# Kernel optimization log

Measured on AMD Instinct MI355X. Metric: run time of the kernel, lower is better.

## Reference

```python
import jax, jax.numpy as jnp
import numpy as np

B, N, C = 4, 256, 256
FH, FW = 100, 152
IMG_H, IMG_W = 800, 1216
SCALE = 0.125          # feature stride 8
POOL, RATIO = 7, 2     # MultiScaleRoIAlign output_size / sampling_ratio
NUM_CLASSES = 91
SCORE_T, NMS_T = 0.05, 0.5
PRE_NMS, DETS = 1024, 100   # fixed-size candidate set for jit-able NMS
WX, WY, WW, WH = 10.0, 10.0, 5.0, 5.0   # bbox_reg_weights
BBOX_CLIP = float(np.log(1000.0 / 16.0))
MIN_SIZE = 1e-2


def setup_inputs():
    key = jax.random.key(0)
    k = jax.random.split(key, 8)
    features = jax.random.normal(k[0], (B, C, FH, FW), jnp.float32)
    p = jax.random.uniform(k[1], (B, N, 4), jnp.float32)
    x1 = jnp.minimum(p[..., 0], p[..., 1]) * (IMG_W - 1.0)
    x2 = jnp.maximum(p[..., 0], p[..., 1]) * (IMG_W - 1.0) + 1.0
    y1 = jnp.minimum(p[..., 2], p[..., 3]) * (IMG_H - 1.0)
    y2 = jnp.maximum(p[..., 2], p[..., 3]) * (IMG_H - 1.0) + 1.0
    proposals = jnp.stack([x1, y1, x2, y2], -1)
    Din = C * POOL * POOL
    W6 = jax.random.normal(k[2], (Din, 1024), jnp.float32) / np.sqrt(Din)
    b6 = jnp.zeros((1024,), jnp.float32)
    W7 = jax.random.normal(k[3], (1024, 1024), jnp.float32) / np.sqrt(1024)
    b7 = jnp.zeros((1024,), jnp.float32)
    Wc = jax.random.normal(k[4], (1024, NUM_CLASSES), jnp.float32) / np.sqrt(1024)
    bc = jnp.zeros((NUM_CLASSES,), jnp.float32)
    Wb = jax.random.normal(k[5], (1024, NUM_CLASSES * 4), jnp.float32) / np.sqrt(1024)
    bb = jnp.zeros((NUM_CLASSES * 4,), jnp.float32)
    return {"features": features, "proposals": proposals, "W6": W6, "b6": b6,
            "W7": W7, "b7": b7, "Wc": Wc, "bc": bc, "Wb": Wb, "bb": bb}


def roi_align(feat, rois, bidx):
    # feat [B,C,H,W]; rois [R,4] in image coords; bidx [R] image index.
    R = rois.shape[0]
    x1, y1 = rois[:, 0] * SCALE, rois[:, 1] * SCALE
    x2, y2 = rois[:, 2] * SCALE, rois[:, 3] * SCALE
    rw = jnp.maximum(x2 - x1, 1.0)
    rh = jnp.maximum(y2 - y1, 1.0)
    off = (jnp.arange(RATIO, dtype=feat.dtype) + 0.5) / RATIO
    grid = (jnp.arange(POOL, dtype=feat.dtype)[:, None] + off[None, :]).reshape(-1)  # [POOL*RATIO]
    gx = jnp.clip(x1[:, None] + (rw / POOL)[:, None] * grid[None, :], 0.0, FW - 1.0)  # [R,14]
    gy = jnp.clip(y1[:, None] + (rh / POOL)[:, None] * grid[None, :], 0.0, FH - 1.0)
    y0 = jnp.floor(gy); x0 = jnp.floor(gx)
    ly = gy - y0; lx = gx - x0
    y0i = jnp.clip(y0, 0, FH - 1).astype(jnp.int32)
    y1i = jnp.clip(y0 + 1.0, 0, FH - 1).astype(jnp.int32)
    x0i = jnp.clip(x0, 0, FW - 1).astype(jnp.int32)
    x1i = jnp.clip(x0 + 1.0, 0, FW - 1).astype(jnp.int32)
    b = bidx[:, None, None]
    def g(yi, xi):  # -> [R, Py, Px, C]
        return feat[b, :, yi[:, :, None], xi[:, None, :]]
    v = ((1 - ly)[:, :, None] * (1 - lx)[:, None, :])[..., None] * g(y0i, x0i) \
      + ((1 - ly)[:, :, None] * lx[:, None, :])[..., None] * g(y0i, x1i) \
      + (ly[:, :, None] * (1 - lx)[:, None, :])[..., None] * g(y1i, x0i) \
      + (ly[:, :, None] * lx[:, None, :])[..., None] * g(y1i, x1i)
    v = v.reshape(R, POOL, RATIO, POOL, RATIO, C).mean((2, 4))  # avg over samples per bin
    return jnp.transpose(v, (0, 3, 1, 2)).reshape(R, C * POOL * POOL)  # channel-major flatten


def decode(deltas, rois):
    # BoxCoder.decode with weights (10,10,5,5); deltas [R,K*4] -> [R,K,4]
    w = rois[:, 2] - rois[:, 0]
    h = rois[:, 3] - rois[:, 1]
    cx = rois[:, 0] + 0.5 * w
    cy = rois[:, 1] + 0.5 * h
    d = deltas.reshape(deltas.shape[0], -1, 4)
    dx, dy = d[..., 0] / WX, d[..., 1] / WY
    dw = jnp.minimum(d[..., 2] / WW, BBOX_CLIP)
    dh = jnp.minimum(d[..., 3] / WH, BBOX_CLIP)
    pcx = dx * w[:, None] + cx[:, None]
    pcy = dy * h[:, None] + cy[:, None]
    pw = jnp.exp(dw) * w[:, None]
    ph = jnp.exp(dh) * h[:, None]
    return jnp.stack([pcx - 0.5 * pw, pcy - 0.5 * ph, pcx + 0.5 * pw, pcy + 0.5 * ph], -1)


def box_iou(a, b):
    area_a = (a[:, 2] - a[:, 0]) * (a[:, 3] - a[:, 1])
    area_b = (b[:, 2] - b[:, 0]) * (b[:, 3] - b[:, 1])
    lt = jnp.maximum(a[:, None, :2], b[None, :, :2])
    rb = jnp.minimum(a[:, None, 2:], b[None, :, 2:])
    wh = jnp.clip(rb - lt, 0.0)
    inter = wh[..., 0] * wh[..., 1]
    return inter / (area_a[:, None] + area_b[None, :] - inter + 1e-9)


def _post(boxes, scores):
    # per-image: boxes [N,K1,4], scores [N,K1] (background already dropped)
    n = boxes.shape[0]
    k1 = boxes.shape[1]
    fb = boxes.reshape(-1, 4)
    fs = scores.reshape(-1)
    labels = jnp.tile(jnp.arange(1, k1 + 1, dtype=jnp.int32), n)
    ws = fb[:, 2] - fb[:, 0]
    hs = fb[:, 3] - fb[:, 1]
    valid = (fs > SCORE_T) & (ws >= MIN_SIZE) & (hs >= MIN_SIZE)
    vals, idx = jax.lax.top_k(jnp.where(valid, fs, -1.0), PRE_NMS)
    cb = fb[idx]
    cl = labels[idx]
    # batched per-class NMS via class offset trick
    ob = cb + (cl.astype(cb.dtype) * (max(IMG_H, IMG_W) + 2.0))[:, None]
    iou = box_iou(ob, ob)
    ar = jnp.arange(PRE_NMS)
    def body(i, keep):
        sup = keep[i] & (iou[i] > NMS_T) & (ar > i)
        return keep & jnp.logical_not(sup)
    keep = jax.lax.fori_loop(0, PRE_NMS, body, vals > SCORE_T)
    sv, oidx = jax.lax.top_k(jnp.where(keep, vals, -1.0), DETS)
    m = sv > SCORE_T
    out_boxes = jnp.where(m[:, None], cb[oidx], 0.0)
    out_scores = jnp.where(m, sv, 0.0)
    out_labels = jnp.where(m, cl[oidx], 0)
    return out_boxes, out_scores, out_labels


def _forward(features, proposals, W6, b6, W7, b7, Wc, bc, Wb, bb):
    rois = proposals.reshape(-1, 4)                     # [R,4]
    bidx = jnp.repeat(jnp.arange(B, dtype=jnp.int32), N)
    x = roi_align(features, rois, bidx)                 # [R, C*49]
    x = jax.nn.relu(x @ W6 + b6)                        # TwoMLPHead fc6
    x = jax.nn.relu(x @ W7 + b7)                        # fc7
    logits = x @ Wc + bc                                # FastRCNNPredictor
    deltas = x @ Wb + bb
    boxes = decode(deltas, rois)                        # [R,K,4]
    boxes = jnp.stack([jnp.clip(boxes[..., 0], 0.0, IMG_W),
                       jnp.clip(boxes[..., 1], 0.0, IMG_H),
                       jnp.clip(boxes[..., 2], 0.0, IMG_W),
                       jnp.clip(boxes[..., 3], 0.0, IMG_H)], -1)
    scores = jax.nn.softmax(logits, -1)
    boxes = boxes[:, 1:].reshape(B, N, NUM_CLASSES - 1, 4)   # drop background class
    scores = scores[:, 1:].reshape(B, N, NUM_CLASSES - 1)
    return jax.vmap(_post)(boxes, scores)


def reference(features, proposals, W6, b6, W7, b7, Wc, bc, Wb, bb):
    # returns (boxes [B,100,4], scores [B,100], labels [B,100])
    return _forward(features, proposals, W6, b6, W7, b7, Wc, bc, Wb, bb)
```

## Files before the change

kernel.cpp:

```cpp
#include <hip/hip_runtime.h>
#include <hip/hip_bf16.h>
#include <stdint.h>

#define B_    4
#define N_    256
#define C_    256
#define FH_   100
#define FW_   152
#define P_HW  (FH_*FW_)
#define NCLS  91
#define CAND  23040
#define DIN   12544
#define PRE   1024

typedef unsigned long long u64;
typedef unsigned int u32;
typedef unsigned short u16;
typedef __attribute__((ext_vector_type(8))) _Float16 half8;
typedef __attribute__((ext_vector_type(8))) short short8;
typedef __attribute__((ext_vector_type(4))) float f32x4;

__device__ inline u16 h2bits(_Float16 h) { return *reinterpret_cast<u16*>(&h); }

__device__ inline void split2(float v, u16& b0, u16& b1) {
  _Float16 h0 = (_Float16)v;
  float r = v - (float)h0;
  _Float16 h1 = (_Float16)r;
  b0 = h2bits(h0); b1 = h2bits(h1);
}

__device__ inline void gload_lds16(const void* g, void* l) {
  __builtin_amdgcn_global_load_lds(
      (const __attribute__((address_space(1))) void*)g,
      (__attribute__((address_space(3))) void*)l, 16, 0, 0);
}

__global__ void k_transpose(const float* __restrict__ in, float* __restrict__ out) {
  __shared__ float t[32][33];
  int b  = blockIdx.z;
  int c0 = blockIdx.y * 32;
  int p0 = blockIdx.x * 32;
  int tx = threadIdx.x & 31, ty = threadIdx.x >> 5;
  const float* inb = in  + (size_t)b * C_ * P_HW;
  float*       ob  = out + (size_t)b * P_HW * C_;
  #pragma unroll
  for (int q = 0; q < 4; q++)
    t[ty + q*8][tx] = inb[(size_t)(c0 + ty + q*8) * P_HW + p0 + tx];
  __syncthreads();
  #pragma unroll
  for (int q = 0; q < 4; q++)
    ob[(size_t)(p0 + ty + q*8) * C_ + c0 + tx] = t[tx][ty + q*8];
}

__global__ void k_packs(const float* __restrict__ W7, u16* __restrict__ W7t,
                        const float* __restrict__ Wc, const float* __restrict__ Wb,
                        const float* __restrict__ bc, const float* __restrict__ bb,
                        u16* __restrict__ Wcatt, float* __restrict__ bcat) {
  int bid = blockIdx.x;
  int tid = threadIdx.x;
  if (bid < 512) {
    int idx = bid * 256 + tid;
    int col = idx & 1023, ko = idx >> 10;
    short8 c0v, c1v;
    #pragma unroll
    for (int e = 0; e < 8; e++) {
      float w = W7[(size_t)(ko*8 + e)*1024 + col] * 128.0f;
      u16 h0, h1;
      split2(w, h0, h1);
      c0v[e] = (short)h0; c1v[e] = (short)h1;
    }
    *reinterpret_cast<short8*>(W7t + ((size_t)ko*1024 + col)*8)         = c0v;
    *reinterpret_cast<short8*>(W7t + ((size_t)(128 + ko)*1024 + col)*8) = c1v;
  } else {
    int idx = (bid - 512) * 256 + tid;
    int col = idx & 511, ko = idx >> 9;
    short8 c0v, c1v;
    #pragma unroll
    for (int e = 0; e < 8; e++) {
      int k = ko*8 + e;
      float w = 0.f;
      if (col < 91)       w = Wc[(size_t)k*91 + col];
      else if (col < 455) w = Wb[(size_t)k*364 + (col - 91)];
      w *= 128.0f;
      u16 h0, h1;
      split2(w, h0, h1);
      c0v[e] = (short)h0; c1v[e] = (short)h1;
    }
    *reinterpret_cast<short8*>(Wcatt + ((size_t)ko*512 + col)*8)         = c0v;
    *reinterpret_cast<short8*>(Wcatt + ((size_t)(128 + ko)*512 + col)*8) = c1v;
    if (idx < 512) {
      float bv = 0.f;
      if (idx < 91)       bv = bc[idx];
      else if (idx < 455) bv = bb[idx - 91];
      bcat[idx] = bv;
    }
  }
}

__global__ __launch_bounds__(256, 8) void k_roialign(const float* __restrict__ featT,
                                                     const float* __restrict__ props,
                                                     u16* __restrict__ Xs) {
  __shared__ float sPW[196][8];
  __shared__ float cellv[32][51];
  int bid = blockIdx.x;
  int xcd = bid & 7;
  int b = xcd >> 1;
  int n = ((bid >> 3) << 1) | (xcd & 1);
  int r = (b << 8) | n;
  int tid = threadIdx.x;

  float x1 = props[r*4+0], y1 = props[r*4+1];
  float x2 = props[r*4+2], y2 = props[r*4+3];
  float x1s = x1 * 0.125f, y1s = y1 * 0.125f;
  float x2s = x2 * 0.125f, y2s = y2 * 0.125f;
  float rw = fmaxf(x2s - x1s, 1.0f);
  float rh = fmaxf(y2s - y1s, 1.0f);
  float rwd = rw / 7.0f, rhd = rh / 7.0f;

  if (tid < 196) {
    int cell = tid >> 2, s = tid & 3;
    int py = cell / 7, px = cell % 7;
    int sy = s >> 1, sx = s & 1;
    float gqy = (float)py + 0.25f + 0.5f * (float)sy;
    float gqx = (float)px + 0.25f + 0.5f * (float)sx;
    float gy = fminf(fmaxf(y1s + rhd * gqy, 0.0f), 99.0f);
    float gx = fminf(fmaxf(x1s + rwd * gqx, 0.0f), 151.0f);
    float y0f = floorf(gy), x0f = floorf(gx);
    float ly = gy - y0f, lx = gx - x0f;
    int y0i = (int)y0f;
    int y1i = (int)fminf(y0f + 1.0f, 99.0f);
    int x0i = (int)x0f;
    int x1i = (int)fminf(x0f + 1.0f, 151.0f);
    sPW[tid][0] = __int_as_float((y0i * FW_ + x0i) * 256);
    sPW[tid][1] = __int_as_float((y0i * FW_ + x1i) * 256);
    sPW[tid][2] = __int_as_float((y1i * FW_ + x0i) * 256);
    sPW[tid][3] = __int_as_float((y1i * FW_ + x1i) * 256);
    sPW[tid][4] = (1.f-ly)*(1.f-lx);
    sPW[tid][5] = (1.f-ly)*lx;
    sPW[tid][6] = ly*(1.f-lx);
    sPW[tid][7] = ly*lx;
  }
  __syncthreads();

  int c32 = tid & 31;
  int slot = tid >> 5;
  const size_t PLS = (size_t)(DIN/8) * 1024 * 8;

  for (int g = 0; g < 8; g++) {
    const float* fb = featT + (size_t)b * P_HW * C_ + g*32 + c32;
    for (int cell = slot; cell < 49; cell += 8) {
      float acc = 0.f;
      #pragma unroll
      for (int s = 0; s < 4; s++) {
        int cs = cell*4 + s;
        float4 pv = *(const float4*)&sPW[cs][0];
        float4 wv = *(const float4*)&sPW[cs][4];
        acc += wv.x * fb[__float_as_int(pv.x)]
             + wv.y * fb[__float_as_int(pv.y)]
             + wv.z * fb[__float_as_int(pv.z)]
             + wv.w * fb[__float_as_int(pv.w)];
      }
      cellv[c32][cell] = acc * 4.0f;
    }
    __syncthreads();
    if (tid < 196) {
      short8 v0, v1;
      #pragma unroll
      for (int e = 0; e < 8; e++) {
        int kl = tid*8 + e;
        int chl = kl / 49;
        int cell = kl - chl*49;
        float v = cellv[chl][cell];
        u16 h0, h1;
        split2(v, h0, h1);
        v0[e] = (short)h0; v1[e] = (short)h1;
      }
      size_t cg = (size_t)g*196 + tid;
      size_t base = (cg * 1024 + r) * 8;
      *reinterpret_cast<short8*>(Xs + base)       = v0;
      *reinterpret_cast<short8*>(Xs + PLS + base) = v1;
    }
    __syncthreads();
  }
}

__global__ __launch_bounds__(512) void k_gemm_f16(
    const u16* __restrict__ As, const float* __restrict__ Bw,
    float* __restrict__ part, int kg, int nsteps, int nct, int outw,
    size_t sstride) {
  __shared__ __align__(16) char lds[65536];
  int tid = threadIdx.x;
  int wid = tid >> 6, lane = tid & 63;
  int l15 = lane & 15, lq = lane >> 4;
  int bid = blockIdx.x;
  int z = bid & 7, xy = bid >> 3;
  int col0 = (xy % nct) * 128, row0 = (xy / nct) * 128;
  int wr = wid >> 2, wc = wid & 3;
  int kbase0 = z * nsteps * 32;

  auto STAGE = [&](int s, int bsel) {
    int kb = kbase0 + s * 32;
    char* dst = lds + bsel * 32768;
    #pragma unroll
    for (int j = 0; j < 4; j++) {
      int cid = tid + j*512;
      const char* src;
      if (j < 2) {
        int pl = cid >> 9;
        int kc = (cid >> 7) & 3, rr = cid & 127;
        src = (const char*)(As + ((size_t)(pl*kg + (kb>>3) + kc)*1024 + row0 + rr)*8);
      } else {
        int cid2 = cid - 1024;
        int kk = cid2 >> 5, c4 = cid2 & 31;
        int col = (c4*4) ^ (((kk >> 3) & 1) << 4);
        src = (const char*)(Bw + (size_t)(kb + kk)*outw + col0 + col);
      }
      gload_lds16(src, dst + (size_t)cid*16);
    }
  };

  f32x4 acc[4][2];
  #pragma unroll
  for (int i = 0; i < 4; i++)
    #pragma unroll
    for (int j = 0; j < 2; j++)
      #pragma unroll
      for (int q = 0; q < 4; q++) acc[i][j][q] = 0.f;

  STAGE(0, 0);
  for (int s = 0; s < nsteps; s++) {
    int cur = s & 1;
    if (s + 1 < nsteps) {
      STAGE(s + 1, cur ^ 1);
      asm volatile("s_waitcnt vmcnt(4)" ::: "memory");
    } else {
      asm volatile("s_waitcnt vmcnt(0)" ::: "memory");
    }
    __builtin_amdgcn_s_barrier();
    __builtin_amdgcn_sched_barrier(0);

    const u16*   Alds = (const u16*)(lds + cur * 32768);
    const float* Blds = (const float*)(lds + cur * 32768 + 16384);

    half8 af[2][4];
    #pragma unroll
    for (int pl = 0; pl < 2; pl++)
      #pragma unroll
      for (int fr = 0; fr < 4; fr++) {
        int chunk = (pl*4 + lq)*128 + wr*64 + fr*16 + l15;
        af[pl][fr] = *reinterpret_cast<const half8*>(&Alds[(size_t)chunk*8]);
      }
    int cxor = (lq & 1) << 4;
    #pragma unroll
    for (int fc = 0; fc < 2; fc++) {
      int colx = (wc*32 + fc*16 + l15) ^ cxor;
      half8 b0, b1;
      #pragma unroll
      for (int j = 0; j < 8; j++) {
        float w = Blds[(lq*8 + j)*128 + colx] * 128.0f;
        _Float16 h0 = (_Float16)w;
        float rres = w - (float)h0;
        b0[j] = h0; b1[j] = (_Float16)rres;
      }
      #pragma unroll
      for (int fr = 0; fr < 4; fr++) {
        acc[fr][fc] = __builtin_amdgcn_mfma_f32_16x16x32_f16(af[0][fr], b0, acc[fr][fc], 0, 0, 0);
        acc[fr][fc] = __builtin_amdgcn_mfma_f32_16x16x32_f16(af[1][fr], b0, acc[fr][fc], 0, 0, 0);
        acc[fr][fc] = __builtin_amdgcn_mfma_f32_16x16x32_f16(af[0][fr], b1, acc[fr][fc], 0, 0, 0);
      }
    }
    __builtin_amdgcn_sched_barrier(0);
    asm volatile("s_waitcnt lgkmcnt(0)" ::: "memory");
    __builtin_amdgcn_s_barrier();
  }

  float* pp = part + (size_t)z * sstride;
  #pragma unroll
  for (int fr = 0; fr < 4; fr++)
    #pragma unroll
    for (int fc = 0; fc < 2; fc++) {
      int col = col0 + wc*32 + fc*16 + l15;
      #pragma unroll
      for (int rr = 0; rr < 4; rr++) {
        int row = row0 + wr*64 + fr*16 + lq*4 + rr;
        pp[(size_t)row*outw + col] = acc[fr][fc][rr];
      }
    }
}

__global__ __launch_bounds__(512) void k_gemm_f16b(
    const u16* __restrict__ As, const u16* __restrict__ Bt,
    float* __restrict__ part, int kgA, int kgB, int nsteps, int nct, int outw,
    size_t sstride) {
  __shared__ __align__(16) char lds[65536];
  int tid = threadIdx.x;
  int wid = tid >> 6, lane = tid & 63;
  int l15 = lane & 15, lq = lane >> 4;
  int bid = blockIdx.x;
  int z = bid & 7, xy = bid >> 3;
  int col0 = (xy % nct) * 128, row0 = (xy / nct) * 128;
  int wr = wid >> 2, wc = wid & 3;
  int kbase0 = z * nsteps * 32;

  auto STAGE = [&](int s, int bsel) {
    int kb = kbase0 + s * 32;
    char* dst = lds + bsel * 32768;
    #pragma unroll
    for (int j = 0; j < 4; j++) {
      int cid = tid + j*512;
      const char* src;
      if (j < 2) {
        int pl = cid >> 9;
        int kc = (cid >> 7) & 3, rr = cid & 127;
        src = (const char*)(As + ((size_t)(pl*kgA + (kb>>3) + kc)*1024 + row0 + rr)*8);
      } else {
        int cid2 = cid - 1024;
        int pl = cid2 >> 9;
        int kc = (cid2 >> 7) & 3, cc = cid2 & 127;
        src = (const char*)(Bt + ((size_t)(pl*kgB + (kb>>3) + kc)*outw + col0 + cc)*8);
      }
      gload_lds16(src, dst + (size_t)cid*16);
    }
  };

  f32x4 acc[4][2];
  #pragma unroll
  for (int i = 0; i < 4; i++)
    #pragma unroll
    for (int j = 0; j < 2; j++)
      #pragma unroll
      for (int q = 0; q < 4; q++) acc[i][j][q] = 0.f;

  STAGE(0, 0);
  for (int s = 0; s < nsteps; s++) {
    int cur = s & 1;
    if (s + 1 < nsteps) {
      STAGE(s + 1, cur ^ 1);
      asm volatile("s_waitcnt vmcnt(4)" ::: "memory");
    } else {
      asm volatile("s_waitcnt vmcnt(0)" ::: "memory");
    }
    __builtin_amdgcn_s_barrier();
    __builtin_amdgcn_sched_barrier(0);

    const u16* Alds = (const u16*)(lds + cur * 32768);
    const u16* Blds = (const u16*)(lds + cur * 32768 + 16384);

    half8 af[2][4];
    #pragma unroll
    for (int pl = 0; pl < 2; pl++)
      #pragma unroll
      for (int fr = 0; fr < 4; fr++) {
        int chunk = (pl*4 + lq)*128 + wr*64 + fr*16 + l15;
        af[pl][fr] = *reinterpret_cast<const half8*>(&Alds[(size_t)chunk*8]);
      }
    #pragma unroll
    for (int fc = 0; fc < 2; fc++) {
      int cc = wc*32 + fc*16 + l15;
      half8 b0 = *reinterpret_cast<const half8*>(&Blds[(size_t)((0*4 + lq)*128 + cc)*8]);
      half8 b1 = *reinterpret_cast<const half8*>(&Blds[(size_t)((1*4 + lq)*128 + cc)*8]);
      #pragma unroll
      for (int fr = 0; fr < 4; fr++) {
        acc[fr][fc] = __builtin_amdgcn_mfma_f32_16x16x32_f16(af[0][fr], b0, acc[fr][fc], 0, 0, 0);
        acc[fr][fc] = __builtin_amdgcn_mfma_f32_16x16x32_f16(af[1][fr], b0, acc[fr][fc], 0, 0, 0);
        acc[fr][fc] = __builtin_amdgcn_mfma_f32_16x16x32_f16(af[0][fr], b1, acc[fr][fc], 0, 0, 0);
      }
    }
    __builtin_amdgcn_sched_barrier(0);
    asm volatile("s_waitcnt lgkmcnt(0)" ::: "memory");
    __builtin_amdgcn_s_barrier();
  }

  float* pp = part + (size_t)z * sstride;
  #pragma unroll
  for (int fr = 0; fr < 4; fr++)
    #pragma unroll
    for (int fc = 0; fc < 2; fc++) {
      int col = col0 + wc*32 + fc*16 + l15;
      #pragma unroll
      for (int rr = 0; rr < 4; rr++) {
        int row = row0 + wr*64 + fr*16 + lq*4 + rr;
        pp[(size_t)row*outw + col] = acc[fr][fc][rr];
      }
    }
}

__global__ void k_reduce_split(const float* __restrict__ part,
                               const float* __restrict__ bias,
                               u16* __restrict__ ys) {
  int idx = blockIdx.x * 256 + threadIdx.x;
  int row = idx >> 7, cg = idx & 127;
  float4 s0 = {0,0,0,0}, s1 = {0,0,0,0};
  #pragma unroll
  for (int s = 0; s < 8; s++) {
    const float4* p = (const float4*)(part + (size_t)s*1048576 + (size_t)row*1024 + cg*8);
    float4 a = p[0], b = p[1];
    s0.x += a.x; s0.y += a.y; s0.z += a.z; s0.w += a.w;
    s1.x += b.x; s1.y += b.y; s1.z += b.z; s1.w += b.w;
  }
  float v[8] = {s0.x, s0.y, s0.z, s0.w, s1.x, s1.y, s1.z, s1.w};
  short8 o0, o1;
  #pragma unroll
  for (int e = 0; e < 8; e++) {
    float x = v[e] * (1.0f/2048.0f) + bias[cg*8 + e];
    x = fmaxf(x, 0.f) * 16.0f;
    u16 h0, h1;
    split2(x, h0, h1);
    o0[e] = (short)h0; o1[e] = (short)h1;
  }
  size_t base = ((size_t)cg * 1024 + row) * 8;
  *reinterpret_cast<short8*>(ys + base)               = o0;
  *reinterpret_cast<short8*>(ys + (size_t)1048576 + base) = o1;
}

__global__ __launch_bounds__(128) void k_headfin(const float* __restrict__ part,
                                                 const float* __restrict__ bcat,
                                                 const float* __restrict__ props,
                                                 float* __restrict__ cboxes,
                                                 u64* __restrict__ keys) {
  __shared__ float sc[512];
  __shared__ float red[128];
  int r = blockIdx.x;
  int j = threadIdx.x;
  int c0 = j * 4;
  float4 v = {0.f, 0.f, 0.f, 0.f};
  #pragma unroll
  for (int s = 0; s < 8; s++) {
    float4 p = *(const float4*)(part + (size_t)s*524288 + (size_t)r*512 + c0);
    v.x += p.x; v.y += p.y; v.z += p.z; v.w += p.w;
  }
  float4 bz = *(const float4*)(bcat + c0);
  sc[c0+0] = v.x * (1.0f/2048.0f) + bz.x;
  sc[c0+1] = v.y * (1.0f/2048.0f) + bz.y;
  sc[c0+2] = v.z * (1.0f/2048.0f) + bz.z;
  sc[c0+3] = v.w * (1.0f/2048.0f) + bz.w;
  __syncthreads();

  float lg = (j < NCLS) ? sc[j] : -3.4e38f;
  red[j] = lg;
  __syncthreads();
  for (int s = 64; s > 0; s >>= 1) {
    if (j < s) red[j] = fmaxf(red[j], red[j+s]);
    __syncthreads();
  }
  float mx = red[0];
  __syncthreads();
  float e = (j < NCLS) ? expf(lg - mx) : 0.f;
  red[j] = e;
  __syncthreads();
  for (int s = 64; s > 0; s >>= 1) {
    if (j < s) red[j] += red[j+s];
    __syncthreads();
  }
  float p = e / red[0];
  if (j >= 1 && j < NCLS) {
    float px1 = props[r*4+0], py1 = props[r*4+1];
    float px2 = props[r*4+2], py2 = props[r*4+3];
    float w = px2 - px1, h = py2 - py1;
    float cx = px1 + 0.5f*w, cy = py1 + 0.5f*h;
    float d0 = sc[91 + j*4 + 0];
    float d1 = sc[91 + j*4 + 1];
    float d2 = sc[91 + j*4 + 2];
    float d3 = sc[91 + j*4 + 3];
    float dx = d0 / 10.0f, dy = d1 / 10.0f;
    float dw = fminf(d2 / 5.0f, 4.135166556742356f);
    float dh = fminf(d3 / 5.0f, 4.135166556742356f);
    float pcx = dx*w + cx, pcy = dy*h + cy;
    float pw = expf(dw)*w, ph = expf(dh)*h;
    float bx1 = fminf(fmaxf(pcx - 0.5f*pw, 0.f), 1216.f);
    float by1 = fminf(fmaxf(pcy - 0.5f*ph, 0.f),  800.f);
    float bx2 = fminf(fmaxf(pcx + 0.5f*pw, 0.f), 1216.f);
    float by2 = fminf(fmaxf(pcy + 0.5f*ph, 0.f),  800.f);
    bool valid = (p > 0.05f) && ((bx2 - bx1) >= 0.01f) && ((by2 - by1) >= 0.01f);
    int b = r >> 8, n = r & 255;
    int cidx = n*90 + (j-1);
    size_t cb = (size_t)b*CAND + cidx;
    cboxes[cb*4+0] = bx1; cboxes[cb*4+1] = by1;
    cboxes[cb*4+2] = bx2; cboxes[cb*4+3] = by2;
    u64 key = 0ull;
    if (valid)
      key = (((u64)__float_as_uint(p)) << 32) | (u32)(~(u32)cidx);
    keys[cb] = key;
  }
}

#define SORTN 4096
__global__ __launch_bounds__(1024) void k_sort(const u64* __restrict__ keys,
                                               u64* __restrict__ sorted) {
  __shared__ u64 sk[SORTN];
  __shared__ int cnt;
  int t = threadIdx.x;
  int b = blockIdx.x >> 1, h = blockIdx.x & 1;
  if (t == 0) cnt = 0;
  __syncthreads();
  const u64* kb = keys + (size_t)b*CAND + (size_t)h*(CAND/2);
  for (int q = 0; q < 12; q++) {
    int idx = t + q*1024;
    if (idx < CAND/2) {
      u64 k = kb[idx];
      if (k) { int pos = atomicAdd(&cnt, 1); sk[pos] = k; }
    }
  }
  __syncthreads();
  int total = cnt;
  for (int s = t; s < SORTN; s += 1024)
    if (s >= total) sk[s] = 0ull;
  __syncthreads();
  for (int k = 2; k <= SORTN; k <<= 1) {
    for (int jj = k >> 1; jj > 0; jj >>= 1) {
      for (int i = t; i < SORTN; i += 1024) {
        int ixj = i ^ jj;
        if (ixj > i) {
          u64 a = sk[i], bb = sk[ixj];
          bool up = ((i & k) == 0);
          if (up ? (a < bb) : (a > bb)) { sk[i] = bb; sk[ixj] = a; }
        }
      }
      __syncthreads();
    }
  }
  sorted[((size_t)b*2 + h)*1024 + t] = sk[t];
}

__global__ __launch_bounds__(1024) void k_nms(const u64* __restrict__ sorted,
                                              const float* __restrict__ cboxes,
                                              float* __restrict__ out) {
  __shared__ u64 m[2048];
  __shared__ float sX1[1024], sY1[1024], sX2[1024], sY2[1024], sAR[1024];
  __shared__ int keepL[1024];
  __shared__ int wsum[16];
  int t = threadIdx.x;
  int b = blockIdx.x;
  m[t]        = sorted[((size_t)b*2 + 0)*1024 + t];
  m[2047 - t] = sorted[((size_t)b*2 + 1)*1024 + t];
  __syncthreads();
  for (int lg = 10; lg >= 0; lg--) {
    int jj = 1 << lg;
    int pos = ((t >> lg) << (lg+1)) + (t & (jj-1));
    u64 a = m[pos], bb = m[pos + jj];
    if (a < bb) { m[pos] = bb; m[pos + jj] = a; }
    __syncthreads();
  }
  u64 key = m[t];
  bool valid = key != 0ull;
  float score = __uint_as_float((u32)(key >> 32));
  u32 cidx = ~((u32)(key & 0xFFFFFFFFu));
  int label = valid ? (int)(cidx % 90u) + 1 : 0;
  float cb0 = 0.f, cb1 = 0.f, cb2 = 0.f, cb3 = 0.f;
  if (valid) {
    size_t cb = ((size_t)b*CAND + cidx) * 4;
    cb0 = cboxes[cb+0]; cb1 = cboxes[cb+1];
    cb2 = cboxes[cb+2]; cb3 = cboxes[cb+3];
  }
  float off = (float)label * 1218.0f;
  float ox1 = cb0 + off, oy1 = cb1 + off;
  float ox2 = cb2 + off, oy2 = cb3 + off;
  float area = (ox2 - ox1) * (oy2 - oy1);
  sX1[t] = ox1; sY1[t] = oy1; sX2[t] = ox2; sY2[t] = oy2; sAR[t] = area;
  keepL[t] = valid ? 1 : 0;
  __syncthreads();

  int wid = t >> 6, lane = t & 63;
  for (int tile = 0; tile < 16; tile++) {
    if (wid == 0) {
      int idx = tile*64 + lane;
      bool kp = keepL[idx] != 0;
      float bx1 = sX1[idx], by1 = sY1[idx], bx2 = sX2[idx], by2 = sY2[idx], ba = sAR[idx];
      u64 alive = __ballot(kp);
      #pragma unroll 1
      for (int i = 0; i < 63; i++) {
        if ((alive >> i) & 1ull) {
          int ii = tile*64 + i;
          float ltx = fmaxf(sX1[ii], bx1), lty = fmaxf(sY1[ii], by1);
          float rbx = fminf(sX2[ii], bx2), rby = fminf(sY2[ii], by2);
          float iw = fmaxf(rbx - ltx, 0.f), ih = fmaxf(rby - lty, 0.f);
          float inter = iw * ih;
          float iou = inter / (sAR[ii] + ba - inter + 1e-9f);
          if (lane > i && iou > 0.5f) kp = false;
        }
        alive = __ballot(kp);
      }
      keepL[idx] = kp ? 1 : 0;
    }
    __syncthreads();
    if (t >= (tile+1)*64) {
      bool kp = keepL[t] != 0;
      if (kp) {
        #pragma unroll 1
        for (int i = tile*64; i < tile*64 + 64; i++) {
          if (keepL[i]) {
            float ltx = fmaxf(sX1[i], ox1), lty = fmaxf(sY1[i], oy1);
            float rbx = fminf(sX2[i], ox2), rby = fminf(sY2[i], oy2);
            float iw = fmaxf(rbx - ltx, 0.f), ih = fmaxf(rby - lty, 0.f);
            float inter = iw * ih;
            float iou = inter / (sAR[i] + area - inter + 1e-9f);
            if (iou > 0.5f) { kp = false; }
          }
        }
        if (!kp) keepL[t] = 0;
      }
    }
    __syncthreads();
  }

  bool keep = keepL[t] != 0;
  u64 bal = __ballot(keep);
  int wpre = __popcll(bal & ((1ull << lane) - 1ull));
  if (lane == 0) wsum[wid] = __popcll(bal);
  __syncthreads();
  int offn = 0, KT = 0;
  for (int q = 0; q < 16; q++) {
    int v = wsum[q];
    if (q < wid) offn += v;
    KT += v;
  }
  int rank = offn + wpre;
  float* outB = out;
  float* outS = out + 1600;
  float* outL = out + 2000;
  if (keep && rank < 100) {
    size_t s = (size_t)b*100 + rank;
    outB[s*4+0] = cb0; outB[s*4+1] = cb1;
    outB[s*4+2] = cb2; outB[s*4+3] = cb3;
    outS[s] = score; outL[s] = (float)label;
  }
  if (t < 100 && t >= KT) {
    size_t s = (size_t)b*100 + t;
    outB[s*4+0] = 0.f; outB[s*4+1] = 0.f; outB[s*4+2] = 0.f; outB[s*4+3] = 0.f;
    outS[s] = 0.f; outL[s] = 0.f;
  }
}

extern "C" void kernel_launch(void* const* d_in, const int* in_sizes, int n_in,
                              void* d_out, int out_size, void* d_ws, size_t ws_size,
                              hipStream_t stream) {
  (void)in_sizes; (void)n_in; (void)out_size; (void)ws_size;
  const float* feat  = (const float*)d_in[0];
  const float* props = (const float*)d_in[1];
  const float* W6 = (const float*)d_in[2];
  const float* b6 = (const float*)d_in[3];
  const float* W7 = (const float*)d_in[4];
  const float* b7 = (const float*)d_in[5];
  const float* Wc = (const float*)d_in[6];
  const float* bc = (const float*)d_in[7];
  const float* Wb = (const float*)d_in[8];
  const float* bb = (const float*)d_in[9];
  float* out = (float*)d_out;
  char* ws = (char*)d_ws;

  float* featT  = (float*)(ws);
  u16*   Xs2    = (u16*)  (ws + 62259200);
  float* part   = (float*)(ws);
  u16*   Y1s2   = (u16*)  (ws + 33554432);
  u16*   Y2s2   = (u16*)  (ws + 37748736);
  u16*   W7t    = (u16*)  (ws + 41943040);
  u16*   Wcatt  = (u16*)  (ws + 46137344);
  float* bcat   = (float*)(ws + 48234496);
  float* cboxes = (float*)(ws + 50102272);
  u64*   keys   = (u64*)  (ws + 51576832);
  u64*   sorted = (u64*)  (ws + 52314112);

  dim3 gT(475, 8, 4);
  k_transpose<<<gT, 256, 0, stream>>>(feat, featT);
  k_roialign<<<1024, 256, 0, stream>>>(featT, props, Xs2);
  k_packs<<<768, 256, 0, stream>>>(W7, W7t, Wc, Wb, bc, bb, Wcatt, bcat);

  k_gemm_f16<<<512, 512, 0, stream>>>(Xs2, W6, part, DIN/8, 49, 8, 1024, 1048576);
  k_reduce_split<<<512, 256, 0, stream>>>(part, b6, Y1s2);
  k_gemm_f16b<<<512, 512, 0, stream>>>(Y1s2, W7t, part, 128, 128, 4, 8, 1024, 1048576);
  k_reduce_split<<<512, 256, 0, stream>>>(part, b7, Y2s2);
  k_gemm_f16b<<<256, 512, 0, stream>>>(Y2s2, Wcatt, part, 128, 128, 4, 4, 512, 524288);
  k_headfin<<<1024, 128, 0, stream>>>(part, bcat, props, cboxes, keys);

  k_sort<<<8, 1024, 0, stream>>>(keys, sorted);
  k_nms<<<4, 1024, 0, stream>>>(sorted, cboxes, out);
}
```

Baseline: 343.6 us.

## Widen fc6 GEMM tile to 128x256 with triple-buffered LDS pipeline

Replaces the generic fc6 split-K GEMM with a specialized kernel using 128x256 output tiles (half the blocks), where each wave covers all rows and a 32-column strip. The f32 W6 tile is read and split into two fp16 halves once per block for twice as many rows, so less conversion work per MFMA. The LDS double buffer becomes a three-stage ring prefetched two steps ahead, with one barrier per step instead of two, and s_setprio raised around the MFMA block. The cost is 144KB of LDS per block and more accumulator registers, leaving one block per CU and fewer blocks to spread across CUs.

```diff
diff --git a/kernel.cpp b/kernel.cpp
--- a/kernel.cpp
+++ b/kernel.cpp
@@ -184,25 +184,23 @@
   }
 }
 
-__global__ __launch_bounds__(512) void k_gemm_f16(
+__global__ __launch_bounds__(512) void k_gemm_fc6(
     const u16* __restrict__ As, const float* __restrict__ Bw,
-    float* __restrict__ part, int kg, int nsteps, int nct, int outw,
-    size_t sstride) {
-  __shared__ __align__(16) char lds[65536];
+    float* __restrict__ part, int kg, int nsteps) {
+  __shared__ __align__(16) char lds[147456];
   int tid = threadIdx.x;
   int wid = tid >> 6, lane = tid & 63;
   int l15 = lane & 15, lq = lane >> 4;
   int bid = blockIdx.x;
   int z = bid & 7, xy = bid >> 3;
-  int col0 = (xy % nct) * 128, row0 = (xy / nct) * 128;
-  int wr = wid >> 2, wc = wid & 3;
+  int col0 = (xy & 3) * 256, row0 = (xy >> 2) * 128;
   int kbase0 = z * nsteps * 32;
 
   auto STAGE = [&](int s, int bsel) {
     int kb = kbase0 + s * 32;
-    char* dst = lds + bsel * 32768;
-    #pragma unroll
-    for (int j = 0; j < 4; j++) {
+    char* dst = lds + (size_t)bsel * 49152;
+    #pragma unroll
+    for (int j = 0; j < 6; j++) {
       int cid = tid + j*512;
       const char* src;
       if (j < 2) {
@@ -211,79 +209,82 @@
         src = (const char*)(As + ((size_t)(pl*kg + (kb>>3) + kc)*1024 + row0 + rr)*8);
       } else {
         int cid2 = cid - 1024;
-        int kk = cid2 >> 5, c4 = cid2 & 31;
+        int kk = cid2 >> 6, c4 = cid2 & 63;
         int col = (c4*4) ^ (((kk >> 3) & 1) << 4);
-        src = (const char*)(Bw + (size_t)(kb + kk)*outw + col0 + col);
+        src = (const char*)(Bw + (size_t)(kb + kk)*1024 + col0 + col);
       }
       gload_lds16(src, dst + (size_t)cid*16);
     }
   };
 
-  f32x4 acc[4][2];
-  #pragma unroll
-  for (int i = 0; i < 4; i++)
+  f32x4 acc[8][2];
+  #pragma unroll
+  for (int i = 0; i < 8; i++)
     #pragma unroll
     for (int j = 0; j < 2; j++)
       #pragma unroll
       for (int q = 0; q < 4; q++) acc[i][j][q] = 0.f;
 
   STAGE(0, 0);
+  if (nsteps > 1) STAGE(1, 1);
+  int rb = 0, tb = 2;
   for (int s = 0; s < nsteps; s++) {
-    int cur = s & 1;
-    if (s + 1 < nsteps) {
-      STAGE(s + 1, cur ^ 1);
-      asm volatile("s_waitcnt vmcnt(4)" ::: "memory");
-    } else {
-      asm volatile("s_waitcnt vmcnt(0)" ::: "memory");
-    }
+    __builtin_amdgcn_sched_barrier(0);
     __builtin_amdgcn_s_barrier();
     __builtin_amdgcn_sched_barrier(0);
-
-    const u16*   Alds = (const u16*)(lds + cur * 32768);
-    const float* Blds = (const float*)(lds + cur * 32768 + 16384);
-
-    half8 af[2][4];
+    if (s + 2 < nsteps) STAGE(s + 2, tb);
+    if (s + 2 < nsteps)      asm volatile("s_waitcnt vmcnt(12)" ::: "memory");
+    else if (s + 1 < nsteps) asm volatile("s_waitcnt vmcnt(6)" ::: "memory");
+    else                     asm volatile("s_waitcnt vmcnt(0)" ::: "memory");
+    __builtin_amdgcn_sched_barrier(0);
+
+    const u16*   Alds = (const u16*)(lds + (size_t)rb * 49152);
+    const float* Blds = (const float*)(lds + (size_t)rb * 49152 + 16384);
+
+    half8 af[2][8];
     #pragma unroll
     for (int pl = 0; pl < 2; pl++)
       #pragma unroll
-      for (int fr = 0; fr < 4; fr++) {
-        int chunk = (pl*4 + lq)*128 + wr*64 + fr*16 + l15;
+      for (int fr = 0; fr < 8; fr++) {
+        int chunk = (pl*4 + lq)*128 + fr*16 + l15;
         af[pl][fr] = *reinterpret_cast<const half8*>(&Alds[(size_t)chunk*8]);
       }
     int cxor = (lq & 1) << 4;
+    __builtin_amdgcn_s_setprio(1);
     #pragma unroll
     for (int fc = 0; fc < 2; fc++) {
-      int colx = (wc*32 + fc*16 + l15) ^ cxor;
+      int colx = (wid*32 + fc*16 + l15) ^ cxor;
       half8 b0, b1;
       #pragma unroll
       for (int j = 0; j < 8; j++) {
-        float w = Blds[(lq*8 + j)*128 + colx] * 128.0f;
+        float w = Blds[(lq*8 + j)*256 + colx] * 128.0f;
         _Float16 h0 = (_Float16)w;
         float rres = w - (float)h0;
         b0[j] = h0; b1[j] = (_Float16)rres;
       }
       #pragma unroll
-      for (int fr = 0; fr < 4; fr++) {
+      for (int fr = 0; fr < 8; fr++) {
         acc[fr][fc] = __builtin_amdgcn_mfma_f32_16x16x32_f16(af[0][fr], b0, acc[fr][fc], 0, 0, 0);
         acc[fr][fc] = __builtin_amdgcn_mfma_f32_16x16x32_f16(af[1][fr], b0, acc[fr][fc], 0, 0, 0);
         acc[fr][fc] = __builtin_amdgcn_mfma_f32_16x16x32_f16(af[0][fr], b1, acc[fr][fc], 0, 0, 0);
       }
     }
+    __builtin_amdgcn_s_setprio(0);
     __builtin_amdgcn_sched_barrier(0);
-    asm volatile("s_waitcnt lgkmcnt(0)" ::: "memory");
-    __builtin_amdgcn_s_barrier();
-  }
-
-  float* pp = part + (size_t)z * sstride;
-  #pragma unroll
-  for (int fr = 0; fr < 4; fr++)
+    rb = (rb == 2) ? 0 : rb + 1;
+    tb = (tb == 2) ? 0 : tb + 1;
+  }
+
+  float* pp = part + (size_t)z * 1048576;
+  #pragma unroll
+  for (int fr = 0; fr < 8; fr++)
     #pragma unroll
     for (int fc = 0; fc < 2; fc++) {
-      int col = col0 + wc*32 + fc*16 + l15;
+      int col = col0 + wid*32 + fc*16 + l15;
       #pragma unroll
       for (int rr = 0; rr < 4; rr++) {
-        int row = row0 + wr*64 + fr*16 + lq*4 + rr;
-        pp[(size_t)row*outw + col] = acc[fr][fc][rr];
+        int row = row0 + fr*16 + lq*4 + rr;
+        pp[(size_t)row*1024 + col] = acc[fr][fc][rr];
       }
     }
 }
@@ -665,7 +666,7 @@
   k_roialign<<<1024, 256, 0, stream>>>(featT, props, Xs2);
   k_packs<<<768, 256, 0, stream>>>(W7, W7t, Wc, Wb, bc, bb, Wcatt, bcat);
 
-  k_gemm_f16<<<512, 512, 0, stream>>>(Xs2, W6, part, DIN/8, 49, 8, 1024, 1048576);
+  k_gemm_fc6<<<256, 512, 0, stream>>>(Xs2, W6, part, DIN/8, 49);
   k_reduce_split<<<512, 256, 0, stream>>>(part, b6, Y1s2);
   k_gemm_f16b<<<512, 512, 0, stream>>>(Y1s2, W7t, part, 128, 128, 4, 8, 1024, 1048576);
   k_reduce_split<<<512, 256, 0, stream>>>(part, b7, Y2s2);
```

After: 337.0 us. Within noise of the previous version (-1.9%).
